# Optimization experiments

Hardware: AMD Instinct MI355X
Metric: run time of the kernel (lower is better)

The kernel has to match this reference:

```python
import jax, jax.numpy as jnp
import numpy as np

B, R, T, D = 16, 1024, 512, 1024
H = 1024  # hidden_dim

def setup_inputs() -> dict:
    key = jax.random.key(0)
    ks = jax.random.split(key, 8)
    s_in = 1.0 / np.sqrt(D)
    s_comb = 1.0 / np.sqrt(3 * D)
    return {
        "region_feats": jax.random.normal(ks[0], (B, R, D), jnp.float32),
        "query_embs": jax.random.normal(ks[1], (B, T, D), jnp.float32),
        "Wr": jax.random.normal(ks[2], (D, H), jnp.float32) * s_in,
        "br": jnp.zeros((H,), jnp.float32),
        "Wq": jax.random.normal(ks[3], (D, H), jnp.float32) * s_in,
        "bq": jnp.zeros((H,), jnp.float32),
        "Ws": jax.random.normal(ks[4], (3 * D, 1), jnp.float32) * s_comb,
        "bs": jnp.zeros((1,), jnp.float32),
    }

def reference(region_feats, query_embs, Wr, br, Wq, bq, Ws, bs):
    # Dense projections
    R_proj = region_feats @ Wr + br            # [B,R,H]
    Q_proj = query_embs @ Wq + bq              # [B,T,H]
    # Unscaled cross-attention scores
    scores = jnp.einsum('brd,btd->brt', R_proj, Q_proj)  # [B,R,T]
    attn = jax.nn.softmax(scores, axis=-1)
    # Attend over RAW query embeddings (as in source)
    attended = jnp.einsum('brt,btd->brd', attn, query_embs)  # [B,R,D]
    combined = jnp.concatenate(
        [region_feats, attended, region_feats * attended], axis=-1)  # [B,R,3D]
    out = combined @ Ws + bs                    # [B,R,1]
    return jnp.squeeze(out, axis=-1)            # [B,R]
```

## Files before the change

kernel.cpp:

```cpp
#include <hip/hip_runtime.h>


#define BD 16
#define RD 1024
#define TD 512
#define DD 1024
#define BR (BD * RD)

typedef _Float16 half8 __attribute__((ext_vector_type(8)));
typedef _Float16 half4 __attribute__((ext_vector_type(4)));
typedef float floatx4 __attribute__((ext_vector_type(4)));

__device__ __forceinline__ float wave_sum(float v) {
#pragma unroll
  for (int off = 32; off > 0; off >>= 1) v += __shfl_down(v, off);
  return v;
}

__device__ __forceinline__ half8 cvt8(float4 a, float4 b) {
  half8 h = {(_Float16)a.x, (_Float16)a.y, (_Float16)a.z, (_Float16)a.w,
             (_Float16)b.x, (_Float16)b.y, (_Float16)b.z, (_Float16)b.w};
  return h;
}

__device__ __forceinline__ void gl16(const _Float16* g, _Float16* l) {
  __builtin_amdgcn_global_load_lds(
      (const __attribute__((address_space(1))) void*)g,
      (__attribute__((address_space(3))) void*)l, 16, 0, 0);
}

#define VMW_(N) asm volatile("s_waitcnt vmcnt(" #N ")" ::: "memory")
#define VMW(N) VMW_(N)
#define BARR                        \
  __builtin_amdgcn_s_barrier();     \
  asm volatile("" ::: "memory")

__global__ __launch_bounds__(256) void prep_all(
    const float* __restrict__ Wr, const float* __restrict__ Wq,
    const float* __restrict__ Ws, const float* __restrict__ br,
    const float* __restrict__ region, const float* __restrict__ query,
    _Float16* __restrict__ M2, _Float16* __restrict__ Ws16,
    float* __restrict__ wqbr, _Float16* __restrict__ wqbr16,
    _Float16* __restrict__ r16, float* __restrict__ rdvec,
    _Float16* __restrict__ q16, float* __restrict__ h1) {
  __shared__ __align__(16) _Float16 lds[2 * 2 * 2048];
  const int blk = blockIdx.x, tid = threadIdx.x;

  if (blk < 256) {
    const int m0 = (blk >> 4) * 64, n0 = (blk & 15) * 64;
    const int lane = tid & 63, w = tid >> 6;
    const int wr = w >> 1, wc = w & 1;
    const int srow = tid >> 2, slot = tid & 3;
    const int scol = (slot ^ ((srow >> 1) & 3)) * 8;
    const long offA = (long)(m0 + srow) * DD + scol;
    const long offB = (long)(n0 + srow) * DD + scol;
    const int wofs = srow * 32 + slot * 8;
    const int NK = DD / 32;
    float4 a0, a1, b0, b1;
    a0 = *(const float4*)(Wr + offA); a1 = *(const float4*)(Wr + offA + 4);
    b0 = *(const float4*)(Wq + offB); b1 = *(const float4*)(Wq + offB + 4);
    *(int4*)&lds[wofs] = *(int4*)&(const half8&)cvt8(a0, a1);
    {
      half8 hb = cvt8(b0, b1);
      *(half8*)&lds[2048 + wofs] = hb;
    }
    a0 = *(const float4*)(Wr + offA + 32); a1 = *(const float4*)(Wr + offA + 36);
    b0 = *(const float4*)(Wq + offB + 32); b1 = *(const float4*)(Wq + offB + 36);
    __syncthreads();
    floatx4 acc[2][2] = {};
    const int fr = lane & 15, g = lane >> 4;
    const int fs = (g ^ ((fr >> 1) & 3)) * 8;
    for (int kt = 0; kt < NK; ++kt) {
      const int cur = (kt & 1) * 4096, nxt = ((kt + 1) & 1) * 4096;
      if (kt + 1 < NK) {
        half8 ha = cvt8(a0, a1), hb = cvt8(b0, b1);
        *(half8*)&lds[nxt + wofs] = ha;
        *(half8*)&lds[nxt + 2048 + wofs] = hb;
      }
      if (kt + 2 < NK) {
        const long go = (long)(kt + 2) * 32;
        a0 = *(const float4*)(Wr + offA + go); a1 = *(const float4*)(Wr + offA + go + 4);
        b0 = *(const float4*)(Wq + offB + go); b1 = *(const float4*)(Wq + offB + go + 4);
      }
      half8 af[2], bf[2];
#pragma unroll
      for (int i = 0; i < 2; ++i)
        af[i] = *(const half8*)&lds[cur + (32 * wr + 16 * i + fr) * 32 + fs];
#pragma unroll
      for (int j = 0; j < 2; ++j)
        bf[j] = *(const half8*)&lds[cur + 2048 + (32 * wc + 16 * j + fr) * 32 + fs];
#pragma unroll
      for (int i = 0; i < 2; ++i)
#pragma unroll
        for (int j = 0; j < 2; ++j)
          acc[i][j] = __builtin_amdgcn_mfma_f32_16x16x32_f16(af[i], bf[j], acc[i][j], 0, 0, 0);
      __syncthreads();
    }
    const int cr = g * 4, cc = fr;
#pragma unroll
    for (int i = 0; i < 2; ++i)
#pragma unroll
      for (int r = 0; r < 4; ++r)
#pragma unroll
        for (int j = 0; j < 2; ++j)
          M2[(long)(m0 + 32 * wr + 16 * i + cr + r) * DD + n0 + 32 * wc + 16 * j + cc] =
              (_Float16)acc[i][j][r];
  } else if (blk < 258) {
    const long i = (long)(blk - 256) * 1024 + tid * 4;
    const float4 v = *(const float4*)&Ws[DD + i];
    half4 h = {(_Float16)v.x, (_Float16)v.y, (_Float16)v.z, (_Float16)v.w};
    *(half4*)&Ws16[i] = h;
  } else if (blk < 514) {
    const int row = (blk - 258) * 4 + (tid >> 6);
    const int lane = tid & 63;
    const float* x = Wq + (long)row * DD;
    float s = 0.f;
    for (int k = lane; k < DD; k += 64) s += x[k] * br[k];
    s = wave_sum(s);
    if (lane == 0) {
      wqbr[row] = s;
      wqbr16[row] = (_Float16)s;
    }
  } else if (blk < 514 + BR / 4) {
    const int wid = tid >> 6, lane = tid & 63;
    const long row = (long)(blk - 514) * 4 + wid;
    const float* src = region + row * DD;
    _Float16* dst = r16 + row * DD;
    float rd = 0.f;
#pragma unroll
    for (int it = 0; it < 4; ++it) {
      const int c = it * 256 + lane * 4;
      const float4 v = *(const float4*)&src[c];
      const float4 w0 = *(const float4*)&Ws[c];
      half4 h = {(_Float16)v.x, (_Float16)v.y, (_Float16)v.z, (_Float16)v.w};
      *(half4*)&dst[c] = h;
      rd += v.x * w0.x + v.y * w0.y + v.z * w0.z + v.w * w0.w;
    }
    rd = wave_sum(rd);
    if (lane == 0) rdvec[row] = rd;
  } else {
    const int wid = tid >> 6, lane = tid & 63;
    const long row = (long)(blk - (514 + BR / 4)) * 4 + wid;
    const float* src = query + row * DD;
    _Float16* dst = q16 + row * DD;
    float hq = 0.f;
#pragma unroll
    for (int it = 0; it < 4; ++it) {
      const int c = it * 256 + lane * 4;
      const float4 v = *(const float4*)&src[c];
      const float4 w1 = *(const float4*)&Ws[DD + c];
      half4 h = {(_Float16)v.x, (_Float16)v.y, (_Float16)v.z, (_Float16)v.w};
      *(half4*)&dst[c] = h;
      hq += v.x * w1.x + v.y * w1.y + v.z * w1.z + v.w * w1.w;
    }
    hq = wave_sum(hq);
    if (lane == 0) h1[row] = hq;
  }
}

#define STAGE2(hh, sl)                                  \
  {                                                     \
    const long go_ = (long)(hh) * 32;                   \
    gl16(gA + go_, &lds[(sl) * 8192 + wbase]);          \
    gl16(gB + go_, &lds[(sl) * 8192 + 4096 + wbase]);   \
  }

#define COMP2(h, sl)                                                           \
  {                                                                            \
    half8 af[2], bf[4];                                                        \
    _Pragma("unroll") for (int i = 0; i < 2; ++i)                              \
      af[i] = *(const half8*)&lds[(sl) * 8192 + (32 * wr + 16 * i + fr) * 32 + fs]; \
    _Pragma("unroll") for (int j = 0; j < 4; ++j)                              \
      bf[j] = *(const half8*)&lds[(sl) * 8192 + 4096 + (64 * wc + 16 * j + fr) * 32 + fs]; \
    if (wc == 0) {                                                             \
      const half8 wb = *(const half8*)&wq_lds[(h) * 32 + g * 8];               \
      _Pragma("unroll") for (int i = 0; i < 2; ++i)                            \
        _Pragma("unroll") for (int e = 0; e < 8; ++e)                          \
          cvp[i] += (float)af[i][e] * (float)wb[e];                            \
    }                                                                          \
    __builtin_amdgcn_s_setprio(1);                                             \
    _Pragma("unroll") for (int i = 0; i < 2; ++i)                              \
      _Pragma("unroll") for (int j = 0; j < 4; ++j)                            \
        acc[i][j] = __builtin_amdgcn_mfma_f32_16x16x32_f16(af[i], bf[j], acc[i][j], 0, 0, 0); \
    __builtin_amdgcn_s_setprio(0);                                             \
  }

__global__ __launch_bounds__(512, 4) void qp_gemm(
    const _Float16* __restrict__ A, const _Float16* __restrict__ B,
    _Float16* __restrict__ C, const _Float16* __restrict__ wq16,
    float* __restrict__ cvec) {
  __shared__ __align__(16) _Float16 lds[4 * 8192];
  __shared__ __align__(16) _Float16 wq_lds[1024];
  const int lin = blockIdx.x;
  const int s = lin & 7, u = lin >> 3;
  const int mt = s * 8 + (u >> 3), nt = u & 7;
  const int m0 = mt * 128, n0 = nt * 128;
  const int tid = threadIdx.x, lane = tid & 63, w = tid >> 6;
  const int wr = w >> 1, wc = w & 1;

  const int lrow = lane >> 2, slot = lane & 3;
  const int scol = (slot ^ ((lrow >> 1) & 3)) * 8;
  const int srow = 16 * w + lrow;
  const _Float16* gA = A + (long)(m0 + srow) * DD + scol;
  const _Float16* gB = B + (long)(n0 + srow) * DD + scol;
  const int wbase = 512 * w;

  if (tid < 128) *(int4*)&wq_lds[tid * 8] = *(const int4*)&wq16[tid * 8];
  __syncthreads();

  floatx4 acc[2][4] = {};
  float cvp[2] = {0.f, 0.f};
  const int fr = lane & 15, g = lane >> 4;
  const int fs = (g ^ ((fr >> 1) & 3)) * 8;

  STAGE2(0, 0); STAGE2(1, 1); STAGE2(2, 2);
  VMW(4); BARR;

  for (int hb = 0; hb < 28; hb += 4) {
    STAGE2(hb + 3, 3); COMP2(hb + 0, 0); VMW(4); BARR;
    STAGE2(hb + 4, 0); COMP2(hb + 1, 1); VMW(4); BARR;
    STAGE2(hb + 5, 1); COMP2(hb + 2, 2); VMW(4); BARR;
    STAGE2(hb + 6, 2); COMP2(hb + 3, 3); VMW(4); BARR;
  }
  STAGE2(31, 3); COMP2(28, 0); VMW(4); BARR;
  COMP2(29, 1); VMW(2); BARR;
  COMP2(30, 2); VMW(0); BARR;
  COMP2(31, 3);

  if (wc == 0 && nt == 0) {
#pragma unroll
    for (int i = 0; i < 2; ++i) {
      float c = cvp[i];
      c += __shfl_xor(c, 16);
      c += __shfl_xor(c, 32);
      if (lane < 16) cvec[m0 + 32 * wr + 16 * i + lane] = c;
    }
  }

  const int cr = g * 4, cc = fr;
#pragma unroll
  for (int i = 0; i < 2; ++i)
#pragma unroll
    for (int r = 0; r < 4; ++r)
#pragma unroll
      for (int j = 0; j < 4; ++j)
        C[(long)(m0 + 32 * wr + 16 * i + cr + r) * DD + n0 + 64 * wc + 16 * j + cc] =
            (_Float16)acc[i][j][r];
}

#define STAGE3(hh, sl)                                    \
  {                                                       \
    const long go_ = (long)(hh) * 32;                     \
    gl16(gA + go_, &lds[(sl) * 12288 + wbase]);           \
    gl16(gP + go_, &lds[(sl) * 12288 + 4096 + wbase]);    \
    gl16(gQ + go_, &lds[(sl) * 12288 + 8192 + wbase]);    \
  }

#define COMP3(h, sl)                                                           \
  {                                                                            \
    half8 af[4], bp[2], bq[2];                                                 \
    _Pragma("unroll") for (int i = 0; i < 4; ++i)                              \
      af[i] = *(const half8*)&lds[(sl) * 12288 + (64 * wr + 16 * i + fr) * 32 + fs]; \
    _Pragma("unroll") for (int j = 0; j < 2; ++j)                              \
      bp[j] = *(const half8*)&lds[(sl) * 12288 + 4096 + (32 * wc + 16 * j + fr) * 32 + fs]; \
    _Pragma("unroll") for (int j = 0; j < 2; ++j)                              \
      bq[j] = *(const half8*)&lds[(sl) * 12288 + 8192 + (32 * wc + 16 * j + fr) * 32 + fs]; \
    const half8 w2f = *(const half8*)&wlds[(h) * 32 + g * 8];                  \
    bq[0] *= w2f;                                                              \
    bq[1] *= w2f;                                                              \
    __builtin_amdgcn_s_setprio(1);                                             \
    _Pragma("unroll") for (int i = 0; i < 4; ++i)                              \
      _Pragma("unroll") for (int j = 0; j < 2; ++j)                            \
        accS[i][j] = __builtin_amdgcn_mfma_f32_16x16x32_f16(af[i], bp[j], accS[i][j], 0, 0, 0); \
    _Pragma("unroll") for (int i = 0; i < 4; ++i)                              \
      _Pragma("unroll") for (int j = 0; j < 2; ++j)                            \
        accH[i][j] = __builtin_amdgcn_mfma_f32_16x16x32_f16(af[i], bq[j], accH[i][j], 0, 0, 0); \
    __builtin_amdgcn_s_setprio(0);                                             \
  }

__global__ __launch_bounds__(512, 4) void gemm_fused(
    const _Float16* __restrict__ A, const _Float16* __restrict__ B0,
    const _Float16* __restrict__ B1,
    float* __restrict__ Ms, float* __restrict__ Ls, float* __restrict__ Hs,
    const float* __restrict__ cvec, const float* __restrict__ h1,
    const _Float16* __restrict__ wsh, long sA, long sB) {
  __shared__ __align__(16) _Float16 lds[3 * 12288];
  __shared__ __align__(16) _Float16 wlds[1024];

  const int lin = blockIdx.x;
  const int s = lin & 7, u = lin >> 3;
  const int b = 2 * s + (u >> 5);
  const int t = u & 31;
  const int mt = t >> 2, nt = t & 3;
  const int m0 = mt * 128, n0 = nt * 128;
  A += (long)b * sA;
  B0 += (long)b * sB;
  B1 += (long)b * sB;

  const int tid = threadIdx.x, lane = tid & 63, w = tid >> 6;
  const int wr = w >> 2, wc = w & 3;

  const int lrow = lane >> 2, slot = lane & 3;
  const int scol = (slot ^ ((lrow >> 1) & 3)) * 8;
  const int srow = 16 * w + lrow;
  const _Float16* gA = A + (long)(m0 + srow) * DD + scol;
  const _Float16* gP = B0 + (long)(n0 + srow) * DD + scol;
  const _Float16* gQ = B1 + (long)(n0 + srow) * DD + scol;
  const int wbase = 512 * w;

  if (tid < 128) *(int4*)&wlds[tid * 8] = *(const int4*)&wsh[1024 + tid * 8];
  __syncthreads();

  floatx4 accS[4][2] = {};
  floatx4 accH[4][2] = {};
  const int fr = lane & 15, g = lane >> 4;
  const int fs = (g ^ ((fr >> 1) & 3)) * 8;

  STAGE3(0, 0); STAGE3(1, 1);
  VMW(3); BARR;

  for (int hb = 0; hb < 30; hb += 3) {
    STAGE3(hb + 2, 2); COMP3(hb + 0, 0); VMW(3); BARR;
    STAGE3(hb + 3, 0); COMP3(hb + 1, 1); VMW(3); BARR;
    STAGE3(hb + 4, 1); COMP3(hb + 2, 2); VMW(3); BARR;
  }
  COMP3(30, 0); VMW(0); BARR;
  COMP3(31, 1);

  const int cr = g * 4, cc = fr;
  float cv[2], hv[2];
#pragma unroll
  for (int j = 0; j < 2; ++j) {
    const long col = (long)b * TD + n0 + 32 * wc + 16 * j + cc;
    cv[j] = cvec[col];
    hv[j] = h1[col];
  }
  const int chunk = nt * 4 + wc;
  const long rowBase = (long)b * RD + m0 + 64 * wr + cr;
#pragma unroll
  for (int i = 0; i < 4; ++i) {
#pragma unroll
    for (int r = 0; r < 4; ++r) {
      float mx = fmaxf(accS[i][0][r] + cv[0], accS[i][1][r] + cv[1]);
      mx = fmaxf(mx, __shfl_xor(mx, 1));
      mx = fmaxf(mx, __shfl_xor(mx, 2));
      mx = fmaxf(mx, __shfl_xor(mx, 4));
      mx = fmaxf(mx, __shfl_xor(mx, 8));
      float l = 0.f, hs = 0.f;
#pragma unroll
      for (int j = 0; j < 2; ++j) {
        const float e = __expf(accS[i][j][r] + cv[j] - mx);
        l += e;
        hs += e * (accH[i][j][r] + hv[j]);
      }
      l += __shfl_xor(l, 1); hs += __shfl_xor(hs, 1);
      l += __shfl_xor(l, 2); hs += __shfl_xor(hs, 2);
      l += __shfl_xor(l, 4); hs += __shfl_xor(hs, 4);
      l += __shfl_xor(l, 8); hs += __shfl_xor(hs, 8);
      if (cc == 0) {
        const long idx = (long)chunk * BR + rowBase + 16 * i + r;
        Ms[idx] = mx;
        Ls[idx] = l;
        Hs[idx] = hs;
      }
    }
  }
}

__global__ __launch_bounds__(256) void combine(
    const float* __restrict__ Ms, const float* __restrict__ Ls,
    const float* __restrict__ Hs, const float* __restrict__ rdvec,
    const float* __restrict__ bs, float* __restrict__ out) {
  const int row = blockIdx.x * 256 + threadIdx.x;
  float mv[16];
  float gm = -1e30f;
#pragma unroll
  for (int c = 0; c < 16; ++c) {
    mv[c] = Ms[(long)c * BR + row];
    gm = fmaxf(gm, mv[c]);
  }
  float L = 0.f, HS = 0.f;
#pragma unroll
  for (int c = 0; c < 16; ++c) {
    const float sc = __expf(mv[c] - gm);
    L += Ls[(long)c * BR + row] * sc;
    HS += Hs[(long)c * BR + row] * sc;
  }
  out[row] = HS / L + rdvec[row] + bs[0];
}

extern "C" void kernel_launch(void* const* d_in, const int* in_sizes, int n_in,
                              void* d_out, int out_size, void* d_ws, size_t ws_size,
                              hipStream_t stream) {
  const float* region = (const float*)d_in[0];
  const float* query  = (const float*)d_in[1];
  const float* Wr     = (const float*)d_in[2];
  const float* br     = (const float*)d_in[3];
  const float* Wq     = (const float*)d_in[4];
  const float* Ws     = (const float*)d_in[6];
  const float* bs     = (const float*)d_in[7];
  float* out = (float*)d_out;

  char* p = (char*)d_ws;
  _Float16* region16 = (_Float16*)p;
  _Float16* query16  = (_Float16*)(p + (32u << 20));
  _Float16* Qp       = (_Float16*)(p + (48u << 20));
  _Float16* M2       = (_Float16*)(p + (64u << 20));
  _Float16* Ws16     = (_Float16*)(p + (66u << 20));
  float*    wqbr     = (float*)(p + (66u << 20) + 8192);
  _Float16* wqbr16   = (_Float16*)(p + (66u << 20) + 12288);
  float*    cvec     = (float*)(p + (66u << 20) + 16384);
  float*    rdvec    = (float*)(p + (66u << 20) + 65536);
  float*    h1       = (float*)(p + (66u << 20) + 131072);
  float*    Ms       = (float*)(p + (67u << 20));
  float*    Ls       = Ms + 16 * BR;
  float*    Hs       = Ls + 16 * BR;

  prep_all<<<dim3(514 + BR / 4 + BD * TD / 4), 256, 0, stream>>>(
      Wr, Wq, Ws, br, region, query, M2, Ws16, wqbr, wqbr16,
      region16, rdvec, query16, h1);
  qp_gemm<<<dim3(512), 512, 0, stream>>>(query16, M2, Qp, wqbr16, cvec);
  gemm_fused<<<dim3(512), 512, 0, stream>>>(
      region16, Qp, query16, Ms, Ls, Hs, cvec, h1, Ws16,
      (long)RD * DD, (long)TD * DD);
  combine<<<dim3(BR / 256), 256, 0, stream>>>(Ms, Ls, Hs, rdvec, bs, out);
}
```

Measured before the change: 216.5 us.

## Fuse combine into gemm_fused via last-block atomic counter; use double-buffered K loop

```diff
diff --git a/kernel.cpp b/kernel.cpp
--- a/kernel.cpp
+++ b/kernel.cpp
@@ -42,7 +42,8 @@
     _Float16* __restrict__ M2, _Float16* __restrict__ Ws16,
     float* __restrict__ wqbr, _Float16* __restrict__ wqbr16,
     _Float16* __restrict__ r16, float* __restrict__ rdvec,
-    _Float16* __restrict__ q16, float* __restrict__ h1) {
+    _Float16* __restrict__ q16, float* __restrict__ h1,
+    int* __restrict__ cnt) {
   __shared__ __align__(16) _Float16 lds[2 * 2 * 2048];
   const int blk = blockIdx.x, tid = threadIdx.x;
 
@@ -110,6 +111,7 @@
     const float4 v = *(const float4*)&Ws[DD + i];
     half4 h = {(_Float16)v.x, (_Float16)v.y, (_Float16)v.z, (_Float16)v.w};
     *(half4*)&Ws16[i] = h;
+    if (blk == 256 && tid < 128) cnt[tid] = 0;
   } else if (blk < 514) {
     const int row = (blk - 258) * 4 + (tid >> 6);
     const int lane = tid & 63;
@@ -248,44 +250,17 @@
             (_Float16)acc[i][j][r];
 }
 
-#define STAGE3(hh, sl)                                    \
-  {                                                       \
-    const long go_ = (long)(hh) * 32;                     \
-    gl16(gA + go_, &lds[(sl) * 12288 + wbase]);           \
-    gl16(gP + go_, &lds[(sl) * 12288 + 4096 + wbase]);    \
-    gl16(gQ + go_, &lds[(sl) * 12288 + 8192 + wbase]);    \
-  }
-
-#define COMP3(h, sl)                                                           \
-  {                                                                            \
-    half8 af[4], bp[2], bq[2];                                                 \
-    _Pragma("unroll") for (int i = 0; i < 4; ++i)                              \
-      af[i] = *(const half8*)&lds[(sl) * 12288 + (64 * wr + 16 * i + fr) * 32 + fs]; \
-    _Pragma("unroll") for (int j = 0; j < 2; ++j)                              \
-      bp[j] = *(const half8*)&lds[(sl) * 12288 + 4096 + (32 * wc + 16 * j + fr) * 32 + fs]; \
-    _Pragma("unroll") for (int j = 0; j < 2; ++j)                              \
-      bq[j] = *(const half8*)&lds[(sl) * 12288 + 8192 + (32 * wc + 16 * j + fr) * 32 + fs]; \
-    const half8 w2f = *(const half8*)&wlds[(h) * 32 + g * 8];                  \
-    bq[0] *= w2f;                                                              \
-    bq[1] *= w2f;                                                              \
-    __builtin_amdgcn_s_setprio(1);                                             \
-    _Pragma("unroll") for (int i = 0; i < 4; ++i)                              \
-      _Pragma("unroll") for (int j = 0; j < 2; ++j)                            \
-        accS[i][j] = __builtin_amdgcn_mfma_f32_16x16x32_f16(af[i], bp[j], accS[i][j], 0, 0, 0); \
-    _Pragma("unroll") for (int i = 0; i < 4; ++i)                              \
-      _Pragma("unroll") for (int j = 0; j < 2; ++j)                            \
-        accH[i][j] = __builtin_amdgcn_mfma_f32_16x16x32_f16(af[i], bq[j], accH[i][j], 0, 0, 0); \
-    __builtin_amdgcn_s_setprio(0);                                             \
-  }
-
 __global__ __launch_bounds__(512, 4) void gemm_fused(
     const _Float16* __restrict__ A, const _Float16* __restrict__ B0,
     const _Float16* __restrict__ B1,
     float* __restrict__ Ms, float* __restrict__ Ls, float* __restrict__ Hs,
     const float* __restrict__ cvec, const float* __restrict__ h1,
-    const _Float16* __restrict__ wsh, long sA, long sB) {
-  __shared__ __align__(16) _Float16 lds[3 * 12288];
+    const _Float16* __restrict__ wsh, const float* __restrict__ rdvec,
+    const float* __restrict__ bs, int* __restrict__ cnt,
+    float* __restrict__ out, long sA, long sB) {
+  __shared__ __align__(16) _Float16 lds[2 * 3 * 4096];
   __shared__ __align__(16) _Float16 wlds[1024];
+  __shared__ int winflag;
 
   const int lin = blockIdx.x;
   const int s = lin & 7, u = lin >> 3;
@@ -309,23 +284,52 @@
   const int wbase = 512 * w;
 
   if (tid < 128) *(int4*)&wlds[tid * 8] = *(const int4*)&wsh[1024 + tid * 8];
+
+  gl16(gA, &lds[wbase]);
+  gl16(gP, &lds[4096 + wbase]);
+  gl16(gQ, &lds[8192 + wbase]);
   __syncthreads();
 
   floatx4 accS[4][2] = {};
   floatx4 accH[4][2] = {};
   const int fr = lane & 15, g = lane >> 4;
   const int fs = (g ^ ((fr >> 1) & 3)) * 8;
-
-  STAGE3(0, 0); STAGE3(1, 1);
-  VMW(3); BARR;
-
-  for (int hb = 0; hb < 30; hb += 3) {
-    STAGE3(hb + 2, 2); COMP3(hb + 0, 0); VMW(3); BARR;
-    STAGE3(hb + 3, 0); COMP3(hb + 1, 1); VMW(3); BARR;
-    STAGE3(hb + 4, 1); COMP3(hb + 2, 2); VMW(3); BARR;
-  }
-  COMP3(30, 0); VMW(0); BARR;
-  COMP3(31, 1);
+  const int NK = DD / 32;
+
+  for (int kt = 0; kt < NK; ++kt) {
+    const int cur = (kt & 1) * 12288;
+    const int nxt = cur ^ 12288;
+    if (kt + 1 < NK) {
+      const long go = (long)(kt + 1) * 32;
+      gl16(gA + go, &lds[nxt + wbase]);
+      gl16(gP + go, &lds[nxt + 4096 + wbase]);
+      gl16(gQ + go, &lds[nxt + 8192 + wbase]);
+    }
+    half8 af[4], bp[2], bq[2];
+#pragma unroll
+    for (int i = 0; i < 4; ++i)
+      af[i] = *(const half8*)&lds[cur + (64 * wr + 16 * i + fr) * 32 + fs];
+#pragma unroll
+    for (int j = 0; j < 2; ++j)
+      bp[j] = *(const half8*)&lds[cur + 4096 + (32 * wc + 16 * j + fr) * 32 + fs];
+#pragma unroll
+    for (int j = 0; j < 2; ++j)
+      bq[j] = *(const half8*)&lds[cur + 8192 + (32 * wc + 16 * j + fr) * 32 + fs];
+    const half8 w2f = *(const half8*)&wlds[kt * 32 + g * 8];
+#pragma unroll
+    for (int j = 0; j < 2; ++j) bq[j] *= w2f;
+#pragma unroll
+    for (int i = 0; i < 4; ++i)
+#pragma unroll
+      for (int j = 0; j < 2; ++j)
+        accS[i][j] = __builtin_amdgcn_mfma_f32_16x16x32_f16(af[i], bp[j], accS[i][j], 0, 0, 0);
+#pragma unroll
+    for (int i = 0; i < 4; ++i)
+#pragma unroll
+      for (int j = 0; j < 2; ++j)
+        accH[i][j] = __builtin_amdgcn_mfma_f32_16x16x32_f16(af[i], bq[j], accH[i][j], 0, 0, 0);
+    __syncthreads();
+  }
 
   const int cr = g * 4, cc = fr;
   float cv[2], hv[2];
@@ -365,28 +369,35 @@
       }
     }
   }
-}
-
-__global__ __launch_bounds__(256) void combine(
-    const float* __restrict__ Ms, const float* __restrict__ Ls,
-    const float* __restrict__ Hs, const float* __restrict__ rdvec,
-    const float* __restrict__ bs, float* __restrict__ out) {
-  const int row = blockIdx.x * 256 + threadIdx.x;
-  float mv[16];
-  float gm = -1e30f;
-#pragma unroll
-  for (int c = 0; c < 16; ++c) {
-    mv[c] = Ms[(long)c * BR + row];
-    gm = fmaxf(gm, mv[c]);
-  }
-  float L = 0.f, HS = 0.f;
-#pragma unroll
-  for (int c = 0; c < 16; ++c) {
-    const float sc = __expf(mv[c] - gm);
-    L += Ls[(long)c * BR + row] * sc;
-    HS += Hs[(long)c * BR + row] * sc;
-  }
-  out[row] = HS / L + rdvec[row] + bs[0];
+
+  __threadfence();
+  __syncthreads();
+  if (tid == 0) winflag = (atomicAdd(&cnt[b * 8 + mt], 1) == 3);
+  __syncthreads();
+  if (winflag) {
+    __threadfence();
+    const int rl = tid >> 2, cq = tid & 3;
+    const long gidx = (long)b * RD + m0 + rl;
+    float mv[4], pm = -1e30f;
+#pragma unroll
+    for (int k = 0; k < 4; ++k) {
+      mv[k] = Ms[(long)(cq * 4 + k) * BR + gidx];
+      pm = fmaxf(pm, mv[k]);
+    }
+    float gm = pm;
+    gm = fmaxf(gm, __shfl_xor(gm, 1));
+    gm = fmaxf(gm, __shfl_xor(gm, 2));
+    float pl = 0.f, ph = 0.f;
+#pragma unroll
+    for (int k = 0; k < 4; ++k) {
+      const float sc = __expf(mv[k] - gm);
+      pl += Ls[(long)(cq * 4 + k) * BR + gidx] * sc;
+      ph += Hs[(long)(cq * 4 + k) * BR + gidx] * sc;
+    }
+    pl += __shfl_xor(pl, 1); ph += __shfl_xor(ph, 1);
+    pl += __shfl_xor(pl, 2); ph += __shfl_xor(ph, 2);
+    if (cq == 0) out[gidx] = ph / pl + rdvec[gidx] + bs[0];
+  }
 }
 
 extern "C" void kernel_launch(void* const* d_in, const int* in_sizes, int n_in,
@@ -412,16 +423,16 @@
   float*    cvec     = (float*)(p + (66u << 20) + 16384);
   float*    rdvec    = (float*)(p + (66u << 20) + 65536);
   float*    h1       = (float*)(p + (66u << 20) + 131072);
+  int*      cnt      = (int*)(p + (66u << 20) + 163840);
   float*    Ms       = (float*)(p + (67u << 20));
   float*    Ls       = Ms + 16 * BR;
   float*    Hs       = Ls + 16 * BR;
 
   prep_all<<<dim3(514 + BR / 4 + BD * TD / 4), 256, 0, stream>>>(
       Wr, Wq, Ws, br, region, query, M2, Ws16, wqbr, wqbr16,
-      region16, rdvec, query16, h1);
+      region16, rdvec, query16, h1, cnt);
   qp_gemm<<<dim3(512), 512, 0, stream>>>(query16, M2, Qp, wqbr16, cvec);
   gemm_fused<<<dim3(512), 512, 0, stream>>>(
-      region16, Qp, query16, Ms, Ls, Hs, cvec, h1, Ws16,
+      region16, Qp, query16, Ms, Ls, Hs, cvec, h1, Ws16, rdvec, bs, cnt, out,
       (long)RD * DD, (long)TD * DD);
-  combine<<<dim3(BR / 256), 256, 0, stream>>>(Ms, Ls, Hs, rdvec, bs, out);
-}
+}
```

After: 318.3 us. +47.0%, slower.
